# Kernel optimization log

Measured on AMD Instinct MI355X. Metric: run time of the kernel, lower is better.

## Reference

```python
import jax, jax.numpy as jnp
import numpy as np

BN_EPS = 1e-5


def _bn(h, gamma, beta, mean, var):
    return (h - mean) * jax.lax.rsqrt(var + BN_EPS) * gamma + beta


def _gin_conv(x, edge_index, edge_weight, Wa, ba, g, be, m, v, Wb, bb):
    # GINConv: (1+eps)*x + sum_j w_ij * x_j, eps=0; then MLP: Linear->BN->ReLU->Linear
    src, dst = edge_index[0], edge_index[1]
    msg = x[src] * edge_weight[:, None]                      # [E, C]
    agg = jax.ops.segment_sum(msg, dst, num_segments=x.shape[0])  # [N, C]
    h = x + agg
    h = h @ Wa + ba
    h = jax.nn.relu(_bn(h, g, be, m, v))
    return h @ Wb + bb


def setup_inputs() -> dict:
    key = jax.random.key(0)
    ks = jax.random.split(key, 16)
    N, E, C_IN, C_OUT, H = 100000, 1600000, 128, 64, 32
    x = jax.random.normal(ks[0], (N, C_IN), dtype=jnp.float32)
    edge_index = jax.random.randint(ks[1], (2, E), 0, N, dtype=jnp.int32)
    edge_weight = jax.random.uniform(ks[2], (E,), dtype=jnp.float32)
    s1 = 1.0 / np.sqrt(C_IN)
    s2 = 1.0 / np.sqrt(H)
    return {
        "x": x,
        "edge_weight": edge_weight,
        "W1a": jax.random.normal(ks[3], (C_IN, H), dtype=jnp.float32) * s1,
        "b1a": jnp.zeros((H,), jnp.float32),
        "g1": jnp.ones((H,), jnp.float32),
        "be1": jnp.zeros((H,), jnp.float32),
        "m1": jax.random.normal(ks[4], (H,), dtype=jnp.float32) * 0.1,
        "v1": jax.random.uniform(ks[5], (H,), dtype=jnp.float32) + 0.5,
        "W1b": jax.random.normal(ks[6], (H, H), dtype=jnp.float32) * s2,
        "b1b": jnp.zeros((H,), jnp.float32),
        "W2a": jax.random.normal(ks[7], (H, C_OUT), dtype=jnp.float32) * s2,
        "b2a": jnp.zeros((C_OUT,), jnp.float32),
        "g2": jnp.ones((C_OUT,), jnp.float32),
        "be2": jnp.zeros((C_OUT,), jnp.float32),
        "m2": jax.random.normal(ks[8], (C_OUT,), dtype=jnp.float32) * 0.1,
        "v2": jax.random.uniform(ks[9], (C_OUT,), dtype=jnp.float32) + 0.5,
        "W2b": jax.random.normal(ks[10], (C_OUT, C_OUT), dtype=jnp.float32) * (1.0 / np.sqrt(C_OUT)),
        "b2b": jnp.zeros((C_OUT,), jnp.float32),
        "edge_index": edge_index,
    }


def reference(x, edge_weight, W1a, b1a, g1, be1, m1, v1, W1b, b1b,
              W2a, b2a, g2, be2, m2, v2, W2b, b2b, edge_index):
    # eval mode: dropout(p=0.6) is identity, BN uses running stats
    h = jax.nn.relu(_gin_conv(x, edge_index, edge_weight,
                              W1a, b1a, g1, be1, m1, v1, W1b, b1b))
    out = _gin_conv(h, edge_index, edge_weight,
                    W2a, b2a, g2, be2, m2, v2, W2b, b2b)
    return out
```

## Files before the change

kernel.cpp:

```cpp
#include <hip/hip_runtime.h>


#define BN_EPS 1e-5f
#define BKT 128
#define BKT_SH 7
#define EPB 4096
#define MAXB 800
#define LDS_E 2560

typedef __attribute__((ext_vector_type(8))) short bf16x8;
typedef __attribute__((ext_vector_type(4))) float f32x4v;

__device__ __forceinline__ unsigned short f2bf(float f) {
    unsigned u = __float_as_uint(f);
    return (unsigned short)((u + 0x7FFFu + ((u >> 16) & 1u)) >> 16);
}
__device__ __forceinline__ float bflo(unsigned u) { return __uint_as_float(u << 16); }
__device__ __forceinline__ float bfhi(unsigned u) { return __uint_as_float(u & 0xFFFF0000u); }

__device__ __forceinline__ void gacc8(uint4 v, float w, float* acc) {
    acc[0] += bflo(v.x) * w; acc[1] += bfhi(v.x) * w;
    acc[2] += bflo(v.y) * w; acc[3] += bfhi(v.y) * w;
    acc[4] += bflo(v.z) * w; acc[5] += bfhi(v.z) * w;
    acc[6] += bflo(v.w) * w; acc[7] += bfhi(v.w) * w;
}

__device__ __forceinline__ void gather_seg8(const unsigned short* __restrict__ tab,
                                            const int2* __restrict__ epack,
                                            int e, int end, int c0, float* acc) {
    long long q0 = 0, q1 = 0, q2 = 0, q3 = 0;
    if (e + 4 <= end) {
        q0 = __builtin_nontemporal_load((const long long*)&epack[e + 0]);
        q1 = __builtin_nontemporal_load((const long long*)&epack[e + 1]);
        q2 = __builtin_nontemporal_load((const long long*)&epack[e + 2]);
        q3 = __builtin_nontemporal_load((const long long*)&epack[e + 3]);
    }
    for (; e + 8 <= end; e += 4) {
        int s0 = (int)q0, s1 = (int)q1, s2 = (int)q2, s3 = (int)q3;
        float w0 = __int_as_float((int)(q0 >> 32));
        float w1 = __int_as_float((int)(q1 >> 32));
        float w2 = __int_as_float((int)(q2 >> 32));
        float w3 = __int_as_float((int)(q3 >> 32));
        uint4 v0 = *(const uint4*)&tab[(size_t)s0 * 32 + c0];
        uint4 v1 = *(const uint4*)&tab[(size_t)s1 * 32 + c0];
        uint4 v2 = *(const uint4*)&tab[(size_t)s2 * 32 + c0];
        uint4 v3 = *(const uint4*)&tab[(size_t)s3 * 32 + c0];
        q0 = __builtin_nontemporal_load((const long long*)&epack[e + 4]);
        q1 = __builtin_nontemporal_load((const long long*)&epack[e + 5]);
        q2 = __builtin_nontemporal_load((const long long*)&epack[e + 6]);
        q3 = __builtin_nontemporal_load((const long long*)&epack[e + 7]);
        gacc8(v0, w0, acc); gacc8(v1, w1, acc);
        gacc8(v2, w2, acc); gacc8(v3, w3, acc);
    }
    if (e + 4 <= end) {
        int s0 = (int)q0, s1 = (int)q1, s2 = (int)q2, s3 = (int)q3;
        float w0 = __int_as_float((int)(q0 >> 32));
        float w1 = __int_as_float((int)(q1 >> 32));
        float w2 = __int_as_float((int)(q2 >> 32));
        float w3 = __int_as_float((int)(q3 >> 32));
        uint4 v0 = *(const uint4*)&tab[(size_t)s0 * 32 + c0];
        uint4 v1 = *(const uint4*)&tab[(size_t)s1 * 32 + c0];
        uint4 v2 = *(const uint4*)&tab[(size_t)s2 * 32 + c0];
        uint4 v3 = *(const uint4*)&tab[(size_t)s3 * 32 + c0];
        gacc8(v0, w0, acc); gacc8(v1, w1, acc);
        gacc8(v2, w2, acc); gacc8(v3, w3, acc);
        e += 4;
    }
    for (; e < end; ++e) {
        long long q = __builtin_nontemporal_load((const long long*)&epack[e]);
        int sn = (int)q;
        float w = __int_as_float((int)(q >> 32));
        uint4 v = *(const uint4*)&tab[(size_t)sn * 32 + c0];
        gacc8(v, w, acc);
    }
}

__global__ __launch_bounds__(256) void gemm1_kernel(const float* __restrict__ x,
                                                    const float* __restrict__ W,
                                                    unsigned short* __restrict__ y1b,
                                                    int* __restrict__ gcur,
                                                    int N, int ncur) {
    __shared__ unsigned short wbT[32][136];
    int t = threadIdx.x;
    if (t == 0) {
        int b0 = blockIdx.x * 16;
        #pragma unroll
        for (int j = 0; j < 16; ++j)
            if (b0 + j < ncur) gcur[b0 + j] = 0;
    }
    for (int i = t; i < 4096; i += 256) {
        int k = i >> 5, c = i & 31;
        wbT[c][k] = f2bf(W[i]);
    }
    __syncthreads();
    int wid = t >> 6, lane = t & 63;
    int lr = lane & 15, lg = lane >> 4;
    int arow = blockIdx.x * 64 + wid * 16 + lr;
    int xr = min(arow, N - 1);
    bf16x8 bf[4][2];
    #pragma unroll
    for (int s = 0; s < 4; ++s) {
        int kb = s * 32 + lg * 8;
        bf[s][0] = *(const bf16x8*)&wbT[lr][kb];
        bf[s][1] = *(const bf16x8*)&wbT[16 + lr][kb];
    }
    f32x4v acc0 = {0.f, 0.f, 0.f, 0.f};
    f32x4v acc1 = {0.f, 0.f, 0.f, 0.f};
    #pragma unroll
    for (int s = 0; s < 4; ++s) {
        const float* xp = &x[(size_t)xr * 128 + s * 32 + lg * 8];
        float4 xa = *(const float4*)xp;
        float4 xb = *(const float4*)(xp + 4);
        bf16x8 af;
        af[0] = (short)f2bf(xa.x); af[1] = (short)f2bf(xa.y);
        af[2] = (short)f2bf(xa.z); af[3] = (short)f2bf(xa.w);
        af[4] = (short)f2bf(xb.x); af[5] = (short)f2bf(xb.y);
        af[6] = (short)f2bf(xb.z); af[7] = (short)f2bf(xb.w);
        acc0 = __builtin_amdgcn_mfma_f32_16x16x32_bf16(af, bf[s][0], acc0, 0, 0, 0);
        acc1 = __builtin_amdgcn_mfma_f32_16x16x32_bf16(af, bf[s][1], acc1, 0, 0, 0);
    }
    int rowbase = blockIdx.x * 64 + wid * 16 + lg * 4;
    #pragma unroll
    for (int r = 0; r < 4; ++r) {
        int orow = rowbase + r;
        if (orow < N) {
            y1b[(size_t)orow * 32 + lr]      = f2bf(acc0[r]);
            y1b[(size_t)orow * 32 + 16 + lr] = f2bf(acc1[r]);
        }
    }
}

__global__ __launch_bounds__(512) void stage_kernel(const int* __restrict__ ei,
                                                    const float* __restrict__ ew,
                                                    int* __restrict__ gcur,
                                                    int2* __restrict__ staged,
                                                    int E, int cap, int NBUCK) {
    __shared__ int hist[MAXB], base_[MAXB], curs[MAXB];
    __shared__ int gbase[MAXB];
    __shared__ int2 data[EPB];
    __shared__ unsigned short bslot[EPB];
    int t  = threadIdx.x;
    int e0 = blockIdx.x * EPB;
    int cnt = min(EPB, E - e0);
    for (int i = t; i < MAXB; i += 512) hist[i] = 0;
    __syncthreads();
    for (int i = t; i < cnt; i += 512) {
        int d = ei[(size_t)E + e0 + i];
        atomicAdd(&hist[d >> BKT_SH], 1);
    }
    __syncthreads();
    int lo = t * 2;
    int v0 = (lo + 0 < MAXB) ? hist[lo + 0] : 0;
    int v1 = (lo + 1 < MAXB) ? hist[lo + 1] : 0;
    int s = v0 + v1;
    gbase[t] = s;
    __syncthreads();
    for (int off = 1; off < 512; off <<= 1) {
        int y = (t >= off) ? gbase[t - off] : 0;
        __syncthreads();
        gbase[t] += y;
        __syncthreads();
    }
    int excl = gbase[t] - s;
    if (lo + 0 < MAXB) { base_[lo + 0] = excl; curs[lo + 0] = excl; }
    excl += v0;
    if (lo + 1 < MAXB) { base_[lo + 1] = excl; curs[lo + 1] = excl; }
    __syncthreads();
    for (int i = t; i < cnt; i += 512) {
        int sn = ei[e0 + i];
        int d  = ei[(size_t)E + e0 + i];
        float w = ew[e0 + i];
        int b = d >> BKT_SH, dl = d & (BKT - 1);
        int pos = atomicAdd(&curs[b], 1);
        data[pos]  = make_int2((dl << 20) | sn, __float_as_int(w));
        bslot[pos] = (unsigned short)b;
    }
    __syncthreads();
    for (int b = t; b < NBUCK; b += 512) {
        int c = hist[b];
        gbase[b] = c ? atomicAdd(&gcur[b * 16], c) : 0;
    }
    __syncthreads();
    for (int i = t; i < cnt; i += 512) {
        int b  = bslot[i];
        int gp = gbase[b] + (i - base_[b]);
        if (gp < cap) staged[(size_t)b * cap + gp] = data[i];
    }
}

__global__ __launch_bounds__(256) void refill_kernel(const int2* __restrict__ staged,
                                                     const int* __restrict__ gcur,
                                                     int2* __restrict__ epack,
                                                     int2* __restrict__ row_se,
                                                     int N, int cap) {
    __shared__ int2 ebuf[LDS_E];
    __shared__ int hist[BKT];
    __shared__ int curs[BKT];
    int b = blockIdx.x, t = threadIdx.x;
    int cnt  = min(gcur[b * 16], cap);
    int base = b * cap;
    size_t e0 = (size_t)b * cap;
    if (t < BKT) hist[t] = 0;
    __syncthreads();
    for (int i = t; i < cnt; i += 256) {
        int2 p = staged[e0 + i];
        ebuf[i] = p;
        atomicAdd(&hist[p.x >> 20], 1);
    }
    __syncthreads();
    if (t < BKT) curs[t] = hist[t];
    __syncthreads();
    for (int off = 1; off < BKT; off <<= 1) {
        int y = (t < BKT && t >= off) ? curs[t - off] : 0;
        __syncthreads();
        if (t < BKT) curs[t] += y;
        __syncthreads();
    }
    if (t < BKT) {
        int excl = curs[t] - hist[t];
        int node = (b << BKT_SH) + t;
        if (node < N) row_se[node] = make_int2(base + excl, base + excl + hist[t]);
        curs[t] = excl;
    }
    __syncthreads();
    for (int i = t; i < cnt; i += 256) {
        int2 p = ebuf[i];
        int dl = p.x >> 20;
        int pos = base + atomicAdd(&curs[dl], 1);
        epack[pos] = make_int2(p.x & 0xFFFFF, p.y);
    }
}

__global__ __launch_bounds__(256) void layer1_kernel(
    const unsigned short* __restrict__ y1b, const int2* __restrict__ row_se,
    const int2* __restrict__ epack,
    const float* __restrict__ b1a, const float* __restrict__ g1,
    const float* __restrict__ be1, const float* __restrict__ m1,
    const float* __restrict__ v1, const float* __restrict__ W1b,
    const float* __restrict__ b1b, unsigned short* __restrict__ h1b, int N) {
    __shared__ float w1b[1024];
    __shared__ float t1s[64][33];
    int t = threadIdx.x;
    for (int i = t; i < 1024; i += 256) w1b[i] = W1b[i];
    __syncthreads();
    int g = t >> 2, l = t & 3;
    int node = blockIdx.x * 64 + g;
    int c0 = l << 3;
    bool act = node < N;
    float acc[8] = {0.f, 0.f, 0.f, 0.f, 0.f, 0.f, 0.f, 0.f};
    if (act) {
        int2 se = row_se[node];
        gather_seg8(y1b, epack, se.x, se.y, c0, acc);
        uint4 sv = *(const uint4*)&y1b[(size_t)node * 32 + c0];
        gacc8(sv, 1.f, acc);
        #pragma unroll
        for (int j = 0; j < 8; ++j) {
            int c = c0 + j;
            float scale = g1[c] * rsqrtf(v1[c] + BN_EPS);
            t1s[g][c] = fmaxf((acc[j] + b1a[c] - m1[c]) * scale + be1[c], 0.f);
        }
    }
    asm volatile("" ::: "memory");
    if (act) {
        float a[8];
        #pragma unroll
        for (int j = 0; j < 8; ++j) a[j] = b1b[c0 + j];
        #pragma unroll
        for (int k = 0; k < 32; ++k) {
            float tv = t1s[g][k];
            const float* wr = &w1b[k * 32 + c0];
            #pragma unroll
            for (int j = 0; j < 8; ++j) a[j] += tv * wr[j];
        }
        unsigned long long p0 = 0, p1 = 0;
        #pragma unroll
        for (int j = 0; j < 4; ++j)
            p0 |= (unsigned long long)f2bf(fmaxf(a[j], 0.f)) << (16 * j);
        #pragma unroll
        for (int j = 0; j < 4; ++j)
            p1 |= (unsigned long long)f2bf(fmaxf(a[4 + j], 0.f)) << (16 * j);
        __builtin_nontemporal_store(p0, (unsigned long long*)&h1b[(size_t)node * 32 + c0 + 0]);
        __builtin_nontemporal_store(p1, (unsigned long long*)&h1b[(size_t)node * 32 + c0 + 4]);
    }
}

__global__ __launch_bounds__(256) void layer2a_kernel(
    const unsigned short* __restrict__ h1b, const int2* __restrict__ row_se,
    const int2* __restrict__ epack,
    const float* __restrict__ W2a, const float* __restrict__ b2a,
    const float* __restrict__ g2, const float* __restrict__ be2,
    const float* __restrict__ m2, const float* __restrict__ v2,
    unsigned short* __restrict__ t2b, int N) {
    __shared__ float w2a[2048];
    __shared__ float s1s[64][33];
    __shared__ float sc2s[64], sh2s[64];
    int t = threadIdx.x;
    for (int i = t; i < 2048; i += 256) w2a[i] = W2a[i];
    if (t < 64) {
        float sc = g2[t] * rsqrtf(v2[t] + BN_EPS);
        sc2s[t] = sc;
        sh2s[t] = (b2a[t] - m2[t]) * sc + be2[t];
    }
    __syncthreads();
    int g = t >> 2, l = t & 3;
    int node = blockIdx.x * 64 + g;
    int c0 = l << 3;
    bool act = node < N;
    float acc[8] = {0.f, 0.f, 0.f, 0.f, 0.f, 0.f, 0.f, 0.f};
    if (act) {
        int2 se = row_se[node];
        gather_seg8(h1b, epack, se.x, se.y, c0, acc);
        uint4 sv = *(const uint4*)&h1b[(size_t)node * 32 + c0];
        gacc8(sv, 1.f, acc);
        #pragma unroll
        for (int j = 0; j < 8; ++j) s1s[g][c0 + j] = acc[j];
    }
    asm volatile("" ::: "memory");
    if (act) {
        int d0 = l << 4;
        float a[16];
        #pragma unroll
        for (int j = 0; j < 16; ++j) a[j] = 0.f;
        #pragma unroll
        for (int k = 0; k < 32; ++k) {
            float sv = s1s[g][k];
            const float* wr = &w2a[k * 64 + d0];
            #pragma unroll
            for (int j = 0; j < 16; ++j) a[j] += sv * wr[j];
        }
        unsigned long long pk[4] = {0, 0, 0, 0};
        #pragma unroll
        for (int j = 0; j < 16; ++j) {
            int c = d0 + j;
            float o = fmaxf(a[j] * sc2s[c] + sh2s[c], 0.f);
            pk[j >> 2] |= (unsigned long long)f2bf(o) << (16 * (j & 3));
        }
        #pragma unroll
        for (int q = 0; q < 4; ++q)
            __builtin_nontemporal_store(pk[q],
                (unsigned long long*)&t2b[(size_t)node * 64 + d0 + 4 * q]);
    }
}

__global__ __launch_bounds__(256) void final_kernel(const unsigned short* __restrict__ t2b,
                                                    const float* __restrict__ W2b,
                                                    const float* __restrict__ b2b,
                                                    float* __restrict__ out, int N) {
    __shared__ float w2b[4096];
    __shared__ float t2s[32][68];
    int t = threadIdx.x;
    for (int i = t; i < 4096; i += 256) w2b[i] = W2b[i];
    int g = t >> 3, l = t & 7;
    int node = blockIdx.x * 32 + g;
    int c0 = l << 3;
    bool act = node < N;
    if (act) {
        uint4 v = *(const uint4*)&t2b[(size_t)node * 64 + c0];
        t2s[g][c0 + 0] = bflo(v.x); t2s[g][c0 + 1] = bfhi(v.x);
        t2s[g][c0 + 2] = bflo(v.y); t2s[g][c0 + 3] = bfhi(v.y);
        t2s[g][c0 + 4] = bflo(v.z); t2s[g][c0 + 5] = bfhi(v.z);
        t2s[g][c0 + 6] = bflo(v.w); t2s[g][c0 + 7] = bfhi(v.w);
    }
    __syncthreads();
    if (act) {
        float a[8];
        #pragma unroll
        for (int j = 0; j < 8; ++j) a[j] = b2b[c0 + j];
        #pragma unroll 8
        for (int k = 0; k < 64; ++k) {
            float tv = t2s[g][k];
            const float* wr = &w2b[k * 64 + c0];
            float4 w0 = *(const float4*)wr;
            float4 w1 = *(const float4*)(wr + 4);
            a[0] += tv * w0.x; a[1] += tv * w0.y; a[2] += tv * w0.z; a[3] += tv * w0.w;
            a[4] += tv * w1.x; a[5] += tv * w1.y; a[6] += tv * w1.z; a[7] += tv * w1.w;
        }
        *(float4*)&out[(size_t)node * 64 + c0 + 0] = *(float4*)&a[0];
        *(float4*)&out[(size_t)node * 64 + c0 + 4] = *(float4*)&a[4];
    }
}

extern "C" void kernel_launch(void* const* d_in, const int* in_sizes, int n_in,
                              void* d_out, int out_size, void* d_ws, size_t ws_size,
                              hipStream_t stream) {
    const float* x   = (const float*)d_in[0];
    const float* ew  = (const float*)d_in[1];
    const float* W1a = (const float*)d_in[2];
    const float* b1a = (const float*)d_in[3];
    const float* g1  = (const float*)d_in[4];
    const float* be1 = (const float*)d_in[5];
    const float* m1  = (const float*)d_in[6];
    const float* v1  = (const float*)d_in[7];
    const float* W1b = (const float*)d_in[8];
    const float* b1b = (const float*)d_in[9];
    const float* W2a = (const float*)d_in[10];
    const float* b2a = (const float*)d_in[11];
    const float* g2  = (const float*)d_in[12];
    const float* be2 = (const float*)d_in[13];
    const float* m2  = (const float*)d_in[14];
    const float* v2  = (const float*)d_in[15];
    const float* W2b = (const float*)d_in[16];
    const float* b2b = (const float*)d_in[17];
    const int*   ei  = (const int*)d_in[18];

    const int N = in_sizes[0] / 128;
    const int E = in_sizes[1];
    const int NBUCK = (N + BKT - 1) >> BKT_SH;
    const int NCUR  = NBUCK * 16;

    unsigned short* y1b = (unsigned short*)d_ws;
    int2*  row_se  = (int2*)(y1b + (size_t)N * 32);
    int*   gcur    = (int*)(row_se + N);
    int2*  epack   = (int2*)(gcur + NCUR + 16);
    size_t fixed_bytes = (char*)epack - (char*)d_ws;
    size_t avail = (ws_size > fixed_bytes) ? (ws_size - fixed_bytes) : 0;
    int cap = (int)((avail / (2 * sizeof(int2))) / NBUCK);
    cap &= ~63;
    if (cap > LDS_E) cap = LDS_E;
    int2* staged = epack + (size_t)NBUCK * cap;
    unsigned short* h1b = (unsigned short*)staged;
    unsigned short* t2b = h1b + (size_t)N * 32;

    gemm1_kernel<<<(N + 63) / 64, 256, 0, stream>>>(x, W1a, y1b, gcur, N, NCUR);
    stage_kernel<<<(E + EPB - 1) / EPB, 512, 0, stream>>>(ei, ew, gcur, staged, E, cap, NBUCK);
    refill_kernel<<<NBUCK, 256, 0, stream>>>(staged, gcur, epack, row_se, N, cap);
    layer1_kernel<<<(N + 63) / 64, 256, 0, stream>>>(y1b, row_se, epack,
                                                     b1a, g1, be1, m1, v1, W1b, b1b, h1b, N);
    layer2a_kernel<<<(N + 63) / 64, 256, 0, stream>>>(h1b, row_se, epack,
                                                      W2a, b2a, g2, be2, m2, v2, t2b, N);
    final_kernel<<<(N + 31) / 32, 256, 0, stream>>>(t2b, W2b, b2b, (float*)d_out, N);
}
```

Baseline: 149.5 us.

## Gather two destination nodes per thread with interleaved edge loads

The layer1 and layer2a kernels now run 128 threads per block, and each thread handles two destination nodes, 32 rows apart. A new dual gather helper interleaves and software-prefetches the edge lists of both nodes, so more independent row loads are in flight per thread. The aim is to hide gather latency through instruction-level parallelism rather than extra waves. The cost is higher register pressure, fewer waves per block, and imbalance when the two nodes have different degrees, with the tail handled by the old single-segment loop.

```diff
diff --git a/kernel.cpp b/kernel.cpp
--- a/kernel.cpp
+++ b/kernel.cpp
@@ -75,6 +75,62 @@
     }
 }
 
+__device__ __forceinline__ void gather_dual(const unsigned short* __restrict__ tab,
+                                            const int2* __restrict__ epack,
+                                            int eA, int endA, int eB, int endB,
+                                            int c0, float* accA, float* accB) {
+    long long a0 = 0, a1 = 0, a2 = 0, a3 = 0;
+    long long b0 = 0, b1 = 0, b2 = 0, b3 = 0;
+    bool pA = eA + 4 <= endA, pB = eB + 4 <= endB;
+    if (pA) {
+        a0 = __builtin_nontemporal_load((const long long*)&epack[eA + 0]);
+        a1 = __builtin_nontemporal_load((const long long*)&epack[eA + 1]);
+        a2 = __builtin_nontemporal_load((const long long*)&epack[eA + 2]);
+        a3 = __builtin_nontemporal_load((const long long*)&epack[eA + 3]);
+    }
+    if (pB) {
+        b0 = __builtin_nontemporal_load((const long long*)&epack[eB + 0]);
+        b1 = __builtin_nontemporal_load((const long long*)&epack[eB + 1]);
+        b2 = __builtin_nontemporal_load((const long long*)&epack[eB + 2]);
+        b3 = __builtin_nontemporal_load((const long long*)&epack[eB + 3]);
+    }
+    while (eA + 8 <= endA && eB + 8 <= endB) {
+        int sa0 = (int)a0, sa1 = (int)a1, sa2 = (int)a2, sa3 = (int)a3;
+        float wa0 = __int_as_float((int)(a0 >> 32));
+        float wa1 = __int_as_float((int)(a1 >> 32));
+        float wa2 = __int_as_float((int)(a2 >> 32));
+        float wa3 = __int_as_float((int)(a3 >> 32));
+        int sb0 = (int)b0, sb1 = (int)b1, sb2 = (int)b2, sb3 = (int)b3;
+        float wb0 = __int_as_float((int)(b0 >> 32));
+        float wb1 = __int_as_float((int)(b1 >> 32));
+        float wb2 = __int_as_float((int)(b2 >> 32));
+        float wb3 = __int_as_float((int)(b3 >> 32));
+        uint4 va0 = *(const uint4*)&tab[(size_t)sa0 * 32 + c0];
+        uint4 va1 = *(const uint4*)&tab[(size_t)sa1 * 32 + c0];
+        uint4 va2 = *(const uint4*)&tab[(size_t)sa2 * 32 + c0];
+        uint4 va3 = *(const uint4*)&tab[(size_t)sa3 * 32 + c0];
+        uint4 vb0 = *(const uint4*)&tab[(size_t)sb0 * 32 + c0];
+        uint4 vb1 = *(const uint4*)&tab[(size_t)sb1 * 32 + c0];
+        uint4 vb2 = *(const uint4*)&tab[(size_t)sb2 * 32 + c0];
+        uint4 vb3 = *(const uint4*)&tab[(size_t)sb3 * 32 + c0];
+        a0 = __builtin_nontemporal_load((const long long*)&epack[eA + 4]);
+        a1 = __builtin_nontemporal_load((const long long*)&epack[eA + 5]);
+        a2 = __builtin_nontemporal_load((const long long*)&epack[eA + 6]);
+        a3 = __builtin_nontemporal_load((const long long*)&epack[eA + 7]);
+        b0 = __builtin_nontemporal_load((const long long*)&epack[eB + 4]);
+        b1 = __builtin_nontemporal_load((const long long*)&epack[eB + 5]);
+        b2 = __builtin_nontemporal_load((const long long*)&epack[eB + 6]);
+        b3 = __builtin_nontemporal_load((const long long*)&epack[eB + 7]);
+        gacc8(va0, wa0, accA); gacc8(va1, wa1, accA);
+        gacc8(va2, wa2, accA); gacc8(va3, wa3, accA);
+        gacc8(vb0, wb0, accB); gacc8(vb1, wb1, accB);
+        gacc8(vb2, wb2, accB); gacc8(vb3, wb3, accB);
+        eA += 4; eB += 4;
+    }
+    gather_seg8(tab, epack, eA, endA, c0, accA);
+    gather_seg8(tab, epack, eB, endB, c0, accB);
+}
+
 __global__ __launch_bounds__(256) void gemm1_kernel(const float* __restrict__ x,
                                                     const float* __restrict__ W,
                                                     unsigned short* __restrict__ y1b,
@@ -231,7 +287,7 @@
     }
 }
 
-__global__ __launch_bounds__(256) void layer1_kernel(
+__global__ __launch_bounds__(128) void layer1_kernel(
     const unsigned short* __restrict__ y1b, const int2* __restrict__ row_se,
     const int2* __restrict__ epack,
     const float* __restrict__ b1a, const float* __restrict__ g1,
@@ -241,50 +297,68 @@
     __shared__ float w1b[1024];
     __shared__ float t1s[64][33];
     int t = threadIdx.x;
-    for (int i = t; i < 1024; i += 256) w1b[i] = W1b[i];
+    for (int i = t; i < 1024; i += 128) w1b[i] = W1b[i];
     __syncthreads();
     int g = t >> 2, l = t & 3;
-    int node = blockIdx.x * 64 + g;
+    int nodeA = blockIdx.x * 64 + g;
+    int nodeB = nodeA + 32;
     int c0 = l << 3;
-    bool act = node < N;
-    float acc[8] = {0.f, 0.f, 0.f, 0.f, 0.f, 0.f, 0.f, 0.f};
-    if (act) {
-        int2 se = row_se[node];
-        gather_seg8(y1b, epack, se.x, se.y, c0, acc);
-        uint4 sv = *(const uint4*)&y1b[(size_t)node * 32 + c0];
-        gacc8(sv, 1.f, acc);
+    bool actA = nodeA < N, actB = nodeB < N;
+    float accA[8] = {0,0,0,0,0,0,0,0};
+    float accB[8] = {0,0,0,0,0,0,0,0};
+    int2 seA = actA ? row_se[nodeA] : make_int2(0, 0);
+    int2 seB = actB ? row_se[nodeB] : make_int2(0, 0);
+    gather_dual(y1b, epack, seA.x, seA.y, seB.x, seB.y, c0, accA, accB);
+    if (actA) {
+        uint4 sv = *(const uint4*)&y1b[(size_t)nodeA * 32 + c0];
+        gacc8(sv, 1.f, accA);
         #pragma unroll
         for (int j = 0; j < 8; ++j) {
             int c = c0 + j;
             float scale = g1[c] * rsqrtf(v1[c] + BN_EPS);
-            t1s[g][c] = fmaxf((acc[j] + b1a[c] - m1[c]) * scale + be1[c], 0.f);
+            t1s[g][c] = fmaxf((accA[j] + b1a[c] - m1[c]) * scale + be1[c], 0.f);
         }
     }
+    if (actB) {
+        uint4 sv = *(const uint4*)&y1b[(size_t)nodeB * 32 + c0];
+        gacc8(sv, 1.f, accB);
+        #pragma unroll
+        for (int j = 0; j < 8; ++j) {
+            int c = c0 + j;
+            float scale = g1[c] * rsqrtf(v1[c] + BN_EPS);
+            t1s[32 + g][c] = fmaxf((accB[j] + b1a[c] - m1[c]) * scale + be1[c], 0.f);
+        }
+    }
     asm volatile("" ::: "memory");
-    if (act) {
-        float a[8];
-        #pragma unroll
-        for (int j = 0; j < 8; ++j) a[j] = b1b[c0 + j];
-        #pragma unroll
-        for (int k = 0; k < 32; ++k) {
-            float tv = t1s[g][k];
-            const float* wr = &w1b[k * 32 + c0];
-            #pragma unroll
-            for (int j = 0; j < 8; ++j) a[j] += tv * wr[j];
+    #pragma unroll
+    for (int half = 0; half < 2; ++half) {
+        int node = half ? nodeB : nodeA;
+        int row  = half ? 32 + g : g;
+        if (node < N) {
+            float a[8];
+            #pragma unroll
+            for (int j = 0; j < 8; ++j) a[j] = b1b[c0 + j];
+            #pragma unroll
+            for (int k = 0; k < 32; ++k) {
+                float tv = t1s[row][k];
+                const float* wr = &w1b[k * 32 + c0];
+                #pragma unroll
+                for (int j = 0; j < 8; ++j) a[j] += tv * wr[j];
+            }
+            unsigned long long p0 = 0, p1 = 0;
+            #pragma unroll
+            for (int j = 0; j < 4; ++j)
+                p0 |= (unsigned long long)f2bf(fmaxf(a[j], 0.f)) << (16 * j);
+            #pragma unroll
+            for (int j = 0; j < 4; ++j)
+                p1 |= (unsigned long long)f2bf(fmaxf(a[4 + j], 0.f)) << (16 * j);
+            __builtin_nontemporal_store(p0, (unsigned long long*)&h1b[(size_t)node * 32 + c0 + 0]);
+            __builtin_nontemporal_store(p1, (unsigned long long*)&h1b[(size_t)node * 32 + c0 + 4]);
         }
-        unsigned long long p0 = 0, p1 = 0;
-        #pragma unroll
-        for (int j = 0; j < 4; ++j)
-            p0 |= (unsigned long long)f2bf(fmaxf(a[j], 0.f)) << (16 * j);
-        #pragma unroll
-        for (int j = 0; j < 4; ++j)
-            p1 |= (unsigned long long)f2bf(fmaxf(a[4 + j], 0.f)) << (16 * j);
-        __builtin_nontemporal_store(p0, (unsigned long long*)&h1b[(size_t)node * 32 + c0 + 0]);
-        __builtin_nontemporal_store(p1, (unsigned long long*)&h1b[(size_t)node * 32 + c0 + 4]);
-    }
-}
-
-__global__ __launch_bounds__(256) void layer2a_kernel(
+    }
+}
+
+__global__ __launch_bounds__(128) void layer2a_kernel(
     const unsigned short* __restrict__ h1b, const int2* __restrict__ row_se,
     const int2* __restrict__ epack,
     const float* __restrict__ W2a, const float* __restrict__ b2a,
@@ -295,7 +369,7 @@
     __shared__ float s1s[64][33];
     __shared__ float sc2s[64], sh2s[64];
     int t = threadIdx.x;
-    for (int i = t; i < 2048; i += 256) w2a[i] = W2a[i];
+    for (int i = t; i < 2048; i += 128) w2a[i] = W2a[i];
     if (t < 64) {
         float sc = g2[t] * rsqrtf(v2[t] + BN_EPS);
         sc2s[t] = sc;
@@ -303,42 +377,56 @@
     }
     __syncthreads();
     int g = t >> 2, l = t & 3;
-    int node = blockIdx.x * 64 + g;
+    int nodeA = blockIdx.x * 64 + g;
+    int nodeB = nodeA + 32;
     int c0 = l << 3;
-    bool act = node < N;
-    float acc[8] = {0.f, 0.f, 0.f, 0.f, 0.f, 0.f, 0.f, 0.f};
-    if (act) {
-        int2 se = row_se[node];
-        gather_seg8(h1b, epack, se.x, se.y, c0, acc);
-        uint4 sv = *(const uint4*)&h1b[(size_t)node * 32 + c0];
-        gacc8(sv, 1.f, acc);
+    bool actA = nodeA < N, actB = nodeB < N;
+    float accA[8] = {0,0,0,0,0,0,0,0};
+    float accB[8] = {0,0,0,0,0,0,0,0};
+    int2 seA = actA ? row_se[nodeA] : make_int2(0, 0);
+    int2 seB = actB ? row_se[nodeB] : make_int2(0, 0);
+    gather_dual(h1b, epack, seA.x, seA.y, seB.x, seB.y, c0, accA, accB);
+    if (actA) {
+        uint4 sv = *(const uint4*)&h1b[(size_t)nodeA * 32 + c0];
+        gacc8(sv, 1.f, accA);
         #pragma unroll
-        for (int j = 0; j < 8; ++j) s1s[g][c0 + j] = acc[j];
+        for (int j = 0; j < 8; ++j) s1s[g][c0 + j] = accA[j];
+    }
+    if (actB) {
+        uint4 sv = *(const uint4*)&h1b[(size_t)nodeB * 32 + c0];
+        gacc8(sv, 1.f, accB);
+        #pragma unroll
+        for (int j = 0; j < 8; ++j) s1s[32 + g][c0 + j] = accB[j];
     }
     asm volatile("" ::: "memory");
-    if (act) {
-        int d0 = l << 4;
-        float a[16];
-        #pragma unroll
-        for (int j = 0; j < 16; ++j) a[j] = 0.f;
-        #pragma unroll
-        for (int k = 0; k < 32; ++k) {
-            float sv = s1s[g][k];
-            const float* wr = &w2a[k * 64 + d0];
-            #pragma unroll
-            for (int j = 0; j < 16; ++j) a[j] += sv * wr[j];
+    int d0 = l << 4;
+    #pragma unroll
+    for (int half = 0; half < 2; ++half) {
+        int node = half ? nodeB : nodeA;
+        int row  = half ? 32 + g : g;
+        if (node < N) {
+            float a[16];
+            #pragma unroll
+            for (int j = 0; j < 16; ++j) a[j] = 0.f;
+            #pragma unroll
+            for (int k = 0; k < 32; ++k) {
+                float sv = s1s[row][k];
+                const float* wr = &w2a[k * 64 + d0];
+                #pragma unroll
+                for (int j = 0; j < 16; ++j) a[j] += sv * wr[j];
+            }
+            unsigned long long pk[4] = {0, 0, 0, 0};
+            #pragma unroll
+            for (int j = 0; j < 16; ++j) {
+                int c = d0 + j;
+                float o = fmaxf(a[j] * sc2s[c] + sh2s[c], 0.f);
+                pk[j >> 2] |= (unsigned long long)f2bf(o) << (16 * (j & 3));
+            }
+            #pragma unroll
+            for (int q = 0; q < 4; ++q)
+                __builtin_nontemporal_store(pk[q],
+                    (unsigned long long*)&t2b[(size_t)node * 64 + d0 + 4 * q]);
         }
-        unsigned long long pk[4] = {0, 0, 0, 0};
-        #pragma unroll
-        for (int j = 0; j < 16; ++j) {
-            int c = d0 + j;
-            float o = fmaxf(a[j] * sc2s[c] + sh2s[c], 0.f);
-            pk[j >> 2] |= (unsigned long long)f2bf(o) << (16 * (j & 3));
-        }
-        #pragma unroll
-        for (int q = 0; q < 4; ++q)
-            __builtin_nontemporal_store(pk[q],
-                (unsigned long long*)&t2b[(size_t)node * 64 + d0 + 4 * q]);
     }
 }
 
@@ -424,9 +512,9 @@
     gemm1_kernel<<<(N + 63) / 64, 256, 0, stream>>>(x, W1a, y1b, gcur, N, NCUR);
     stage_kernel<<<(E + EPB - 1) / EPB, 512, 0, stream>>>(ei, ew, gcur, staged, E, cap, NBUCK);
     refill_kernel<<<NBUCK, 256, 0, stream>>>(staged, gcur, epack, row_se, N, cap);
-    layer1_kernel<<<(N + 63) / 64, 256, 0, stream>>>(y1b, row_se, epack,
+    layer1_kernel<<<(N + 63) / 64, 128, 0, stream>>>(y1b, row_se, epack,
                                                      b1a, g1, be1, m1, v1, W1b, b1b, h1b, N);
-    layer2a_kernel<<<(N + 63) / 64, 256, 0, stream>>>(h1b, row_se, epack,
+    layer2a_kernel<<<(N + 63) / 64, 128, 0, stream>>>(h1b, row_se, epack,
                                                       W2a, b2a, g2, be2, m2, v2, t2b, N);
     final_kernel<<<(N + 31) / 32, 256, 0, stream>>>(t2b, W2b, b2b, (float*)d_out, N);
 }
```

Measured after the change: 162.5 us. 1.09x slower.
